# Performance work log

Measured on AMD Instinct MI355X. Metric: run time of the kernel, lower is better.

Reference implementation:

```python
import jax, jax.numpy as jnp
import numpy as np

N_ELEC = 8192   # electrons (nodes)
N_NUC = 512     # nuclei
EMB = 256       # embedding_dim
KER = 256       # kernel_dim
DF = 64         # dist_feat_dim
MID = 128       # round(sqrt(DF*KER)), log-interpolated hidden width of w-MLP
E = 131072      # edges per edge type


def _ssp(x):
    # shifted softplus, deepqmc default activation: log(0.5*exp(x) + 0.5)
    return jax.nn.softplus(x) - jnp.log(2.0)


def setup_inputs() -> dict:
    key = jax.random.key(0)
    ks = jax.random.split(key, 24)
    def nrm(k, shape, scale):
        return jax.random.normal(k, shape, dtype=jnp.float32) * scale
    inp = {}
    inp['electrons'] = nrm(ks[0], (N_ELEC, EMB), 1.0)
    inp['nuclei'] = nrm(ks[1], (N_NUC, KER), 1.0)
    for i, lbl in enumerate(['same', 'anti', 'n']):
        inp[f'dist_{lbl}'] = jax.random.uniform(ks[2 + i], (E, DF), dtype=jnp.float32)
        inp[f'w1_{lbl}'] = nrm(ks[5 + i], (DF, MID), DF ** -0.5)
        inp[f'b1_{lbl}'] = jnp.zeros((MID,), jnp.float32)
        inp[f'w2_{lbl}'] = nrm(ks[8 + i], (MID, KER), MID ** -0.5)
        inp[f'g_{lbl}'] = nrm(ks[11 + i], (KER, EMB), KER ** -0.5)
    inp['h_w'] = nrm(ks[14], (EMB, KER), EMB ** -0.5)
    inp['senders_same'] = jax.random.randint(ks[15], (E,), 0, N_ELEC)
    inp['senders_anti'] = jax.random.randint(ks[16], (E,), 0, N_ELEC)
    inp['senders_n'] = jax.random.randint(ks[17], (E,), 0, N_NUC)
    inp['receivers_same'] = jax.random.randint(ks[18], (E,), 0, N_ELEC)
    inp['receivers_anti'] = jax.random.randint(ks[19], (E,), 0, N_ELEC)
    inp['receivers_n'] = jax.random.randint(ks[20], (E,), 0, N_ELEC)
    return inp


def reference(electrons, nuclei, dist_same, dist_anti, dist_n,
              w1_same, b1_same, w2_same, w1_anti, b1_anti, w2_anti,
              w1_n, b1_n, w2_n, g_same, g_anti, g_n, h_w,
              senders_same, senders_anti, senders_n,
              receivers_same, receivers_anti, receivers_n):
    def w_mlp(d, w1, b1, w2):
        # MLP with ('log', 2) hidden layers: linear+bias -> SSP -> last linear (no bias)
        return _ssp(d @ w1 + b1) @ w2

    # per-edge filters from distance features: [E, KER]
    we_same = w_mlp(dist_same, w1_same, b1_same, w2_same)
    we_anti = w_mlp(dist_anti, w1_anti, b1_anti, w2_anti)
    we_n = w_mlp(dist_n, w1_n, b1_n, w2_n)

    # shared h (single bias-free linear) on gathered sender electrons: [E, KER]
    hx_same = electrons[senders_same] @ h_w
    hx_anti = electrons[senders_anti] @ h_w

    weh_same = we_same * hx_same
    weh_anti = we_anti * hx_anti
    weh_n = we_n * nuclei[senders_n]

    # scatter-sum messages to receiver electrons: [N_ELEC, KER]
    z_same = jax.ops.segment_sum(weh_same, receivers_same, num_segments=N_ELEC)
    z_anti = jax.ops.segment_sum(weh_anti, receivers_anti, num_segments=N_ELEC)
    z_n = jax.ops.segment_sum(weh_n, receivers_n, num_segments=N_ELEC)

    # per-label g (single bias-free linear) + residual update, order matches original
    return electrons + (z_n @ g_n + z_same @ g_same + z_anti @ g_anti)
```

## Files before the change

### kernel.cpp

```cpp
#include <hip/hip_runtime.h>
#include <stdint.h>


#define N_ELEC 8192
#define N_NUC  512
#define EMB    256
#define KER    256
#define DF     64
#define MID    128
#define NEDGE  131072
#define RPS    8256
#define CSTR   272

using u16 = unsigned short;
typedef short short8 __attribute__((ext_vector_type(8)));
typedef float f32x4 __attribute__((ext_vector_type(4)));

__device__ __forceinline__ float bf2f(u16 h) {
  return __uint_as_float(((unsigned)h) << 16);
}
__device__ __forceinline__ u16 f2bf(float f) {
  unsigned u = __float_as_uint(f);
  return (u16)((u + 0x7FFFu + ((u >> 16) & 1u)) >> 16);
}
__device__ __forceinline__ unsigned pkbf(float a, float b) {
  return ((unsigned)f2bf(b) << 16) | (unsigned)f2bf(a);
}
__device__ __forceinline__ float ssp_fast(float x) {
  const float e = __expf(-fabsf(x));
  return fmaxf(x, 0.f) + __logf(fmaf(0.5f, e, 0.5f));
}

__device__ __forceinline__ void stage_tile(const char* g0, long stride,
                                           char* lds, int tid) {
  const int l = tid & 63, w = tid >> 6;
#pragma unroll
  for (int c = 0; c < 2; ++c) {
    const int r = c * 64 + w * 16 + (l >> 2);
    const int cb = (l & 3) * 16;
    const char* g = g0 + (long)r * stride + cb;
    char* dst = lds + c * 4096 + w * 1024;
    __builtin_amdgcn_global_load_lds(
        (const __attribute__((address_space(1))) unsigned*)g,
        (__attribute__((address_space(3))) unsigned*)dst, 16, 0, 0);
  }
}

__device__ __forceinline__ void stage_f32(const float* g0, int stride_e,
                                          int kt, char* lds, int tid) {
#pragma unroll
  for (int k = 0; k < 8; ++k) {
    const int idx2 = k * 256 + tid;
    const int row = idx2 >> 4, cp = idx2 & 15;
    const float2 v = *(const float2*)(g0 + (long)row * stride_e + kt + cp * 2);
    *(unsigned*)(lds + row * 64 + cp * 4) = pkbf(v.x, v.y);
  }
}

template <bool A_F32>
__device__ __forceinline__ void gemm_core(const char* A0, long as_bytes,
                                          const float* Af, int as_elems,
                                          const char* B0, long bs, int K,
                                          char* As, char* Bs, f32x4 acc[4][4],
                                          int tid) {
  const int l = tid & 63, lane15 = l & 15, quad = l >> 4, wv = tid >> 6;
  const int mw = (wv >> 1) * 64, nw = (wv & 1) * 64;
  for (int kt = 0; kt < K; kt += 32) {
    if (A_F32)
      stage_f32(Af, as_elems, kt, As, tid);
    else
      stage_tile(A0 + (long)kt * 2, as_bytes, As, tid);
    stage_tile(B0 + (long)kt * 2, bs, Bs, tid);
    __syncthreads();
    short8 af[4], bf[4];
#pragma unroll
    for (int i = 0; i < 4; ++i) {
      af[i] = *(const short8*)(As + (mw + i * 16 + lane15) * 64 + quad * 16);
      bf[i] = *(const short8*)(Bs + (nw + i * 16 + lane15) * 64 + quad * 16);
    }
#pragma unroll
    for (int mi = 0; mi < 4; ++mi)
#pragma unroll
      for (int ni = 0; ni < 4; ++ni)
        acc[mi][ni] = __builtin_amdgcn_mfma_f32_16x16x32_bf16(
            af[mi], bf[ni], acc[mi][ni], 0, 0, 0);
    __syncthreads();
  }
}

__device__ __forceinline__ void zero_acc(f32x4 acc[4][4]) {
#pragma unroll
  for (int i = 0; i < 4; ++i)
#pragma unroll
    for (int j = 0; j < 4; ++j) acc[i][j] = (f32x4){0.f, 0.f, 0.f, 0.f};
}

__global__ __launch_bounds__(256) void k_zero2(float4* z, int* cnt) {
  const int b = blockIdx.x;
  if (b < 6144)
    z[b * 256 + threadIdx.x] = (float4){0.f, 0.f, 0.f, 0.f};
  else
    cnt[(b - 6144) * 256 + threadIdx.x] = 0;
}

__global__ __launch_bounds__(256) void k_hist(const int* r0, const int* r1,
                                              const int* r2, int* cnt) {
  const int t = blockIdx.z;
  const int* rcv = t == 0 ? r0 : (t == 1 ? r1 : r2);
  const int e = blockIdx.x * 256 + threadIdx.x;
  atomicAdd(&cnt[t * N_ELEC + rcv[e]], 1);
}

__global__ __launch_bounds__(256) void k_scan(const int* cnt, int* rowptr,
                                              int* cursor) {
  const int t = blockIdx.x, tid = threadIdx.x;
  __shared__ int part[256];
  const int* c = cnt + t * N_ELEC;
  int s = 0;
#pragma unroll
  for (int i = 0; i < 32; ++i) s += c[tid * 32 + i];
  part[tid] = s;
  __syncthreads();
  for (int off = 1; off < 256; off <<= 1) {
    int v = (tid >= off) ? part[tid - off] : 0;
    __syncthreads();
    part[tid] += v;
    __syncthreads();
  }
  int run = (tid == 0) ? 0 : part[tid - 1];
  int* rp = rowptr + t * RPS;
  int* cu = cursor + t * N_ELEC;
  for (int i = 0; i < 32; ++i) {
    rp[tid * 32 + i] = run;
    cu[tid * 32 + i] = run;
    run += c[tid * 32 + i];
  }
  if (tid == 255) rp[N_ELEC] = run;
}

__global__ __launch_bounds__(256) void k_place(const int* r0, const int* r1,
                                               const int* r2, const int* s0,
                                               const int* s1, const int* s2,
                                               int* cursor, int* perm,
                                               int* snd_s, int* rcv_s) {
  const int t = blockIdx.z;
  const int* rcv = t == 0 ? r0 : (t == 1 ? r1 : r2);
  const int* snd = t == 0 ? s0 : (t == 1 ? s1 : s2);
  const int e = blockIdx.x * 256 + threadIdx.x;
  const int rr = rcv[e];
  const int pos = atomicAdd(&cursor[t * N_ELEC + rr], 1);
  perm[t * NEDGE + pos] = e;
  snd_s[t * NEDGE + pos] = snd[e];
  rcv_s[t * NEDGE + pos] = rr;
}

__global__ __launch_bounds__(256) void k_prep(
    const float* h_w, const float* w1s, const float* w1a, const float* w1n,
    const float* w2s, const float* w2a, const float* w2n, const float* gs,
    const float* ga, const float* gn, u16* hwT, u16* w1T, u16* w2T, u16* gT) {
  int i = blockIdx.x * 256 + threadIdx.x;
  if (i < 65536) {
    int n = i >> 8, k = i & 255;
    hwT[i] = f2bf(h_w[k * 256 + n]);
    return;
  }
  int j = i - 65536;
  if (j < 24576) {
    int t = j >> 13, jj = j & 8191, n = jj >> 6, k = jj & 63;
    const float* w1 = t == 0 ? w1s : (t == 1 ? w1a : w1n);
    w1T[j] = f2bf(w1[k * 128 + n]);
    return;
  }
  j -= 24576;
  if (j < 98304) {
    int t = j >> 15, jj = j & 32767, n = jj >> 7, k = jj & 127;
    const float* w2 = t == 0 ? w2s : (t == 1 ? w2a : w2n);
    w2T[j] = f2bf(w2[k * 256 + n]);
    return;
  }
  j -= 98304;
  if (j < 196608) {
    int n = j / 768, q = j % 768, t = q >> 8, k = q & 255;
    const float* g = t == 0 ? gs : (t == 1 ? ga : gn);
    gT[j] = f2bf(g[k * 256 + n]);
  }
}

__global__ __launch_bounds__(256) void k_he(const float* elec, const u16* hwT,
                                            u16* he) {
  __shared__ char As[8192], Bs[8192];
  f32x4 acc[4][4];
  zero_acc(acc);
  const int m0 = blockIdx.x * 128, n0 = blockIdx.y * 128;
  gemm_core<true>(nullptr, 0, elec + (long)m0 * 256, 256,
                  (const char*)hwT + (long)n0 * 512, 512, 256, As, Bs, acc,
                  threadIdx.x);
  const int l = threadIdx.x & 63, lane15 = l & 15, quad = l >> 4,
            wv = threadIdx.x >> 6;
  const int mw = (wv >> 1) * 64, nw = (wv & 1) * 64;
#pragma unroll
  for (int mi = 0; mi < 4; ++mi)
#pragma unroll
    for (int r = 0; r < 4; ++r) {
      const int row = m0 + mw + mi * 16 + quad * 4 + r;
#pragma unroll
      for (int ni = 0; ni < 4; ++ni) {
        const int col = n0 + nw + ni * 16 + lane15;
        he[row * 256 + col] = f2bf(acc[mi][ni][r]);
      }
    }
}

__global__ __launch_bounds__(256) void k_edge(
    const float* d0, const float* d1, const float* d2, const float* b0,
    const float* b1p, const float* b2, const u16* w1T, const u16* w2T,
    const u16* he, const float* nucf, const int* perm, const int* snd_s,
    const int* rcv_s, float* z) {
  __shared__ char mid[128 * CSTR];
  __shared__ char buf[128 * CSTR];
  __shared__ int snd_l[128], rcv_l[128];

  const int t = blockIdx.z;
  const int m0 = blockIdx.x * 128;
  const int tid = threadIdx.x;
  const float* dist = t == 0 ? d0 : (t == 1 ? d1 : d2);
  const float* bias = t == 0 ? b0 : (t == 1 ? b1p : b2);
  const u16* w1t = w1T + t * 8192;
  const u16* w2t = w2T + t * 32768;
  const bool is_nuc = (t == 2);

  if (tid < 128)
    snd_l[tid] = snd_s[t * NEDGE + m0 + tid];
  else
    rcv_l[tid - 128] = rcv_s[t * NEDGE + m0 + tid - 128];

  int rows[4];
  const int* pm = perm + t * NEDGE + m0;
#pragma unroll
  for (int s = 0; s < 4; ++s) rows[s] = pm[(s * 256 + tid) >> 3];
#pragma unroll
  for (int j = 0; j < 2; ++j)
#pragma unroll
    for (int s = 0; s < 4; ++s) {
      const int idx = s * 256 + tid, row = idx >> 3, ch = idx & 7;
      const float4 v =
          *(const float4*)(dist + (long)rows[s] * 64 + j * 32 + ch * 4);
      uint2 p;
      p.x = pkbf(v.x, v.y);
      p.y = pkbf(v.z, v.w);
      *(uint2*)(buf + j * 8192 + row * 64 + ch * 8) = p;
    }
  __syncthreads();

  const int l = tid & 63, lane15 = l & 15, quad = l >> 4, wv = tid >> 6;
  const int mw = (wv >> 1) * 64, nw = (wv & 1) * 64;

  f32x4 acc[4][4];
  zero_acc(acc);
#pragma unroll
  for (int j = 0; j < 2; ++j) {
    short8 af[4], bf[4];
#pragma unroll
    for (int i = 0; i < 4; ++i) {
      af[i] = *(const short8*)(buf + j * 8192 + (mw + i * 16 + lane15) * 64 +
                               quad * 16);
      bf[i] = *(const short8*)(w1t + (nw + i * 16 + lane15) * 64 + j * 32 +
                               quad * 8);
    }
#pragma unroll
    for (int mi = 0; mi < 4; ++mi)
#pragma unroll
      for (int ni = 0; ni < 4; ++ni)
        acc[mi][ni] = __builtin_amdgcn_mfma_f32_16x16x32_bf16(
            af[mi], bf[ni], acc[mi][ni], 0, 0, 0);
  }
  __syncthreads();

#pragma unroll
  for (int mi = 0; mi < 4; ++mi)
#pragma unroll
    for (int r = 0; r < 4; ++r) {
      const int row = mw + mi * 16 + quad * 4 + r;
#pragma unroll
      for (int ni = 0; ni < 4; ++ni) {
        const int col = nw + ni * 16 + lane15;
        const float x = acc[mi][ni][r] + bias[col];
        *(u16*)(mid + row * CSTR + col * 2) = f2bf(ssp_fast(x));
      }
    }
  __syncthreads();

  u16* HeC = (u16*)buf;
  for (int n0 = 0; n0 < 256; n0 += 128) {
    zero_acc(acc);
#pragma unroll
    for (int kt = 0; kt < 128; kt += 32) {
      short8 af[4], bf[4];
#pragma unroll
      for (int i = 0; i < 4; ++i) {
        af[i] = *(const short8*)(mid + (mw + i * 16 + lane15) * CSTR + kt * 2 +
                                 quad * 16);
        bf[i] = *(const short8*)(w2t + (n0 + nw + i * 16 + lane15) * 128 + kt +
                                 quad * 8);
      }
#pragma unroll
      for (int mi = 0; mi < 4; ++mi)
#pragma unroll
        for (int ni = 0; ni < 4; ++ni)
          acc[mi][ni] = __builtin_amdgcn_mfma_f32_16x16x32_bf16(
              af[mi], bf[ni], acc[mi][ni], 0, 0, 0);
    }

    if (!is_nuc) {
#pragma unroll
      for (int c = 0; c < 8; ++c) {
        const int chunk = c * 256 + tid;
        const int row = chunk >> 4, off = chunk & 15;
        const uint4 v = *(const uint4*)((const char*)he +
                                        (size_t)snd_l[row] * 512 + n0 * 2 +
                                        off * 16);
        *(uint4*)((char*)HeC + row * CSTR + off * 16) = v;
      }
    } else {
#pragma unroll
      for (int c = 0; c < 8; ++c) {
        const int chunk = c * 256 + tid;
        const int row = chunk >> 4, off = chunk & 15;
        const char* src =
            (const char*)nucf + (size_t)snd_l[row] * 1024 + n0 * 4 + off * 32;
        const float4 a = *(const float4*)src;
        const float4 b = *(const float4*)(src + 16);
        uint4 p;
        p.x = pkbf(a.x, a.y);
        p.y = pkbf(a.z, a.w);
        p.z = pkbf(b.x, b.y);
        p.w = pkbf(b.z, b.w);
        *(uint4*)((char*)HeC + row * CSTR + off * 16) = p;
      }
    }
    __syncthreads();

#pragma unroll
    for (int mi = 0; mi < 4; ++mi)
#pragma unroll
      for (int r = 0; r < 4; ++r) {
        const int row = mw + mi * 16 + quad * 4 + r;
#pragma unroll
        for (int ni = 0; ni < 4; ++ni) {
          const int col = nw + ni * 16 + lane15;
          u16* p = (u16*)((char*)HeC + row * CSTR) + col;
          *p = f2bf(acc[mi][ni][r] * bf2f(*p));
        }
      }
    __syncthreads();

    {
      const int cp = l;
      const int rbeg = wv * 32, rend = rbeg + 32;
      float a0 = 0.f, a1 = 0.f;
      int cur = rcv_l[rbeg];
      for (int row = rbeg; row < rend; ++row) {
        const unsigned p = *(const unsigned*)((char*)HeC + row * CSTR + cp * 4);
        a0 += __uint_as_float(p << 16);
        a1 += __uint_as_float(p & 0xffff0000u);
        const int nxt = (row + 1 < rend) ? rcv_l[row + 1] : -1;
        if (nxt != cur) {
          float* zp = z + (size_t)cur * 768 + t * 256 + n0 + cp * 2;
          unsafeAtomicAdd(zp, a0);
          unsafeAtomicAdd(zp + 1, a1);
          a0 = a1 = 0.f;
          cur = nxt;
        }
      }
    }
    __syncthreads();
  }
}

__global__ __launch_bounds__(256) void k_final(const float* z, const u16* gT,
                                               const float* elec, float* out) {
  __shared__ char As[8192], Bs[8192];
  f32x4 acc[4][4];
  zero_acc(acc);
  const int m0 = blockIdx.x * 128, n0 = blockIdx.y * 128;
  gemm_core<true>(nullptr, 0, z + (long)m0 * 768, 768,
                  (const char*)gT + (long)n0 * 1536, 1536, 768, As, Bs, acc,
                  threadIdx.x);
  const int l = threadIdx.x & 63, lane15 = l & 15, quad = l >> 4,
            wv = threadIdx.x >> 6;
  const int mw = (wv >> 1) * 64, nw = (wv & 1) * 64;
#pragma unroll
  for (int mi = 0; mi < 4; ++mi)
#pragma unroll
    for (int r = 0; r < 4; ++r) {
      const int row = m0 + mw + mi * 16 + quad * 4 + r;
#pragma unroll
      for (int ni = 0; ni < 4; ++ni) {
        const int col = n0 + nw + ni * 16 + lane15;
        out[row * 256 + col] = acc[mi][ni][r] + elec[row * 256 + col];
      }
    }
}

extern "C" void kernel_launch(void* const* d_in, const int* in_sizes, int n_in,
                              void* d_out, int out_size, void* d_ws,
                              size_t ws_size, hipStream_t stream) {
  int I_dist[3], I_w1[3], I_b1[3], I_w2[3], I_g[3], I_hw;
  if (in_sizes[3] == 64 * 128) {
    for (int t = 0; t < 3; ++t) {
      I_dist[t] = 2 + t * 5 + 0;
      I_w1[t] = 2 + t * 5 + 1;
      I_b1[t] = 2 + t * 5 + 2;
      I_w2[t] = 2 + t * 5 + 3;
      I_g[t] = 2 + t * 5 + 4;
    }
    I_hw = 17;
  } else {
    I_dist[0] = 2; I_dist[1] = 3; I_dist[2] = 4;
    I_w1[0] = 5;  I_b1[0] = 6;  I_w2[0] = 7;
    I_w1[1] = 8;  I_b1[1] = 9;  I_w2[1] = 10;
    I_w1[2] = 11; I_b1[2] = 12; I_w2[2] = 13;
    I_g[0] = 14; I_g[1] = 15; I_g[2] = 16;
    I_hw = 17;
  }
  const int I_snd[3] = {18, 19, 20};
  const int I_rcv[3] = {21, 22, 23};

  char* ws = (char*)d_ws;
  u16* he = (u16*)(ws + 0);
  u16* hwT = (u16*)(ws + 4194304);
  u16* w1T = (u16*)(ws + 4325376);
  u16* w2T = (u16*)(ws + 4374528);
  u16* gT = (u16*)(ws + 4571136);
  float* z = (float*)(ws + 4964352);
  int* cnt = (int*)(ws + 30130176);
  int* rowptr = (int*)(ws + 30228480);
  int* cursor = (int*)(ws + 30327552);
  int* perm = (int*)(ws + 30425856);
  int* snd_s = (int*)(ws + 31998720);
  int* rcv_s = (int*)(ws + 33571584);

  const float* elec = (const float*)d_in[0];
  const float* nuc = (const float*)d_in[1];
  const int* s0 = (const int*)d_in[I_snd[0]];
  const int* s1 = (const int*)d_in[I_snd[1]];
  const int* s2 = (const int*)d_in[I_snd[2]];
  const int* r0 = (const int*)d_in[I_rcv[0]];
  const int* r1 = (const int*)d_in[I_rcv[1]];
  const int* r2 = (const int*)d_in[I_rcv[2]];

  k_zero2<<<6240, 256, 0, stream>>>((float4*)z, cnt);

  k_hist<<<dim3(NEDGE / 256, 1, 3), 256, 0, stream>>>(r0, r1, r2, cnt);
  k_scan<<<3, 256, 0, stream>>>(cnt, rowptr, cursor);
  k_place<<<dim3(NEDGE / 256, 1, 3), 256, 0, stream>>>(r0, r1, r2, s0, s1, s2,
                                                       cursor, perm, snd_s,
                                                       rcv_s);

  k_prep<<<1504, 256, 0, stream>>>(
      (const float*)d_in[I_hw], (const float*)d_in[I_w1[0]],
      (const float*)d_in[I_w1[1]], (const float*)d_in[I_w1[2]],
      (const float*)d_in[I_w2[0]], (const float*)d_in[I_w2[1]],
      (const float*)d_in[I_w2[2]], (const float*)d_in[I_g[0]],
      (const float*)d_in[I_g[1]], (const float*)d_in[I_g[2]], hwT, w1T, w2T,
      gT);

  k_he<<<dim3(N_ELEC / 128, 2), 256, 0, stream>>>(elec, hwT, he);

  k_edge<<<dim3(NEDGE / 128, 1, 3), 256, 0, stream>>>(
      (const float*)d_in[I_dist[0]], (const float*)d_in[I_dist[1]],
      (const float*)d_in[I_dist[2]], (const float*)d_in[I_b1[0]],
      (const float*)d_in[I_b1[1]], (const float*)d_in[I_b1[2]], w1T, w2T, he,
      nuc, perm, snd_s, rcv_s, z);

  k_final<<<dim3(N_ELEC / 128, 2), 256, 0, stream>>>(z, gT, elec,
                                                     (float*)d_out);
}
```

Measured before the change: 436.1 us.

## Shrink dense GEMM tiles to 64x64 and cut edge kernel LDS for occupancy

The k_he and k_final GEMMs move from 128x128 to 64x64 tiles, so each launch has four times as many blocks and uses less shared memory per block, which fills more CUs on the 8192-row problems. In k_edge the separate `mid` LDS buffer is removed: the hidden SSP activations are written into `buf`, preloaded into registers (afr) and reused across both n0 halves. A launch bound of 3 blocks per SM is also added. The aim is higher occupancy and less LDS traffic. The cost is more register pressure from holding the A fragments, and less data reuse per block in the smaller GEMM tiles.

```diff
diff --git a/kernel.cpp b/kernel.cpp
--- a/kernel.cpp
+++ b/kernel.cpp
@@ -31,68 +31,56 @@
   return fmaxf(x, 0.f) + __logf(fmaf(0.5f, e, 0.5f));
 }
 
-__device__ __forceinline__ void stage_tile(const char* g0, long stride,
-                                           char* lds, int tid) {
+__device__ __forceinline__ void stage_t64(const char* g0, long stride,
+                                          char* lds, int tid) {
   const int l = tid & 63, w = tid >> 6;
-#pragma unroll
-  for (int c = 0; c < 2; ++c) {
-    const int r = c * 64 + w * 16 + (l >> 2);
-    const int cb = (l & 3) * 16;
-    const char* g = g0 + (long)r * stride + cb;
-    char* dst = lds + c * 4096 + w * 1024;
-    __builtin_amdgcn_global_load_lds(
-        (const __attribute__((address_space(1))) unsigned*)g,
-        (__attribute__((address_space(3))) unsigned*)dst, 16, 0, 0);
-  }
-}
-
-__device__ __forceinline__ void stage_f32(const float* g0, int stride_e,
+  const int r = w * 16 + (l >> 2);
+  const int cb = (l & 3) * 16;
+  __builtin_amdgcn_global_load_lds(
+      (const __attribute__((address_space(1))) unsigned*)(g0 +
+                                                          (long)r * stride +
+                                                          cb),
+      (__attribute__((address_space(3))) unsigned*)(lds + w * 1024), 16, 0, 0);
+}
+__device__ __forceinline__ void stage_f64(const float* g0, int stride_e,
                                           int kt, char* lds, int tid) {
 #pragma unroll
-  for (int k = 0; k < 8; ++k) {
+  for (int k = 0; k < 4; ++k) {
     const int idx2 = k * 256 + tid;
     const int row = idx2 >> 4, cp = idx2 & 15;
     const float2 v = *(const float2*)(g0 + (long)row * stride_e + kt + cp * 2);
     *(unsigned*)(lds + row * 64 + cp * 4) = pkbf(v.x, v.y);
   }
 }
-
 template <bool A_F32>
-__device__ __forceinline__ void gemm_core(const char* A0, long as_bytes,
-                                          const float* Af, int as_elems,
-                                          const char* B0, long bs, int K,
-                                          char* As, char* Bs, f32x4 acc[4][4],
-                                          int tid) {
+__device__ __forceinline__ void gemm64(const char* A0, long as_bytes,
+                                       const float* Af, int as_elems,
+                                       const char* B0, long bs, int K,
+                                       char* As, char* Bs, f32x4 acc[2][2],
+                                       int tid) {
   const int l = tid & 63, lane15 = l & 15, quad = l >> 4, wv = tid >> 6;
-  const int mw = (wv >> 1) * 64, nw = (wv & 1) * 64;
+  const int mw = (wv >> 1) * 32, nw = (wv & 1) * 32;
   for (int kt = 0; kt < K; kt += 32) {
     if (A_F32)
-      stage_f32(Af, as_elems, kt, As, tid);
+      stage_f64(Af, as_elems, kt, As, tid);
     else
-      stage_tile(A0 + (long)kt * 2, as_bytes, As, tid);
-    stage_tile(B0 + (long)kt * 2, bs, Bs, tid);
-    __syncthreads();
-    short8 af[4], bf[4];
-#pragma unroll
-    for (int i = 0; i < 4; ++i) {
+      stage_t64(A0 + (long)kt * 2, as_bytes, As, tid);
+    stage_t64(B0 + (long)kt * 2, bs, Bs, tid);
+    __syncthreads();
+    short8 af[2], bf[2];
+#pragma unroll
+    for (int i = 0; i < 2; ++i) {
       af[i] = *(const short8*)(As + (mw + i * 16 + lane15) * 64 + quad * 16);
       bf[i] = *(const short8*)(Bs + (nw + i * 16 + lane15) * 64 + quad * 16);
     }
 #pragma unroll
-    for (int mi = 0; mi < 4; ++mi)
-#pragma unroll
-      for (int ni = 0; ni < 4; ++ni)
+    for (int mi = 0; mi < 2; ++mi)
+#pragma unroll
+      for (int ni = 0; ni < 2; ++ni)
         acc[mi][ni] = __builtin_amdgcn_mfma_f32_16x16x32_bf16(
             af[mi], bf[ni], acc[mi][ni], 0, 0, 0);
     __syncthreads();
   }
-}
-
-__device__ __forceinline__ void zero_acc(f32x4 acc[4][4]) {
-#pragma unroll
-  for (int i = 0; i < 4; ++i)
-#pragma unroll
-    for (int j = 0; j < 4; ++j) acc[i][j] = (f32x4){0.f, 0.f, 0.f, 0.f};
 }
 
 __global__ __launch_bounds__(256) void k_zero2(float4* z, int* cnt) {
@@ -188,35 +176,37 @@
 
 __global__ __launch_bounds__(256) void k_he(const float* elec, const u16* hwT,
                                             u16* he) {
-  __shared__ char As[8192], Bs[8192];
-  f32x4 acc[4][4];
-  zero_acc(acc);
-  const int m0 = blockIdx.x * 128, n0 = blockIdx.y * 128;
-  gemm_core<true>(nullptr, 0, elec + (long)m0 * 256, 256,
-                  (const char*)hwT + (long)n0 * 512, 512, 256, As, Bs, acc,
-                  threadIdx.x);
+  __shared__ char As[4096], Bs[4096];
+  f32x4 acc[2][2];
+#pragma unroll
+  for (int i = 0; i < 2; ++i)
+#pragma unroll
+    for (int j = 0; j < 2; ++j) acc[i][j] = (f32x4){0.f, 0.f, 0.f, 0.f};
+  const int m0 = blockIdx.x * 64, n0 = blockIdx.y * 64;
+  gemm64<true>(nullptr, 0, elec + (long)m0 * 256, 256,
+               (const char*)hwT + (long)n0 * 512, 512, 256, As, Bs, acc,
+               threadIdx.x);
   const int l = threadIdx.x & 63, lane15 = l & 15, quad = l >> 4,
             wv = threadIdx.x >> 6;
-  const int mw = (wv >> 1) * 64, nw = (wv & 1) * 64;
-#pragma unroll
-  for (int mi = 0; mi < 4; ++mi)
+  const int mw = (wv >> 1) * 32, nw = (wv & 1) * 32;
+#pragma unroll
+  for (int mi = 0; mi < 2; ++mi)
 #pragma unroll
     for (int r = 0; r < 4; ++r) {
       const int row = m0 + mw + mi * 16 + quad * 4 + r;
 #pragma unroll
-      for (int ni = 0; ni < 4; ++ni) {
+      for (int ni = 0; ni < 2; ++ni) {
         const int col = n0 + nw + ni * 16 + lane15;
         he[row * 256 + col] = f2bf(acc[mi][ni][r]);
       }
     }
 }
 
-__global__ __launch_bounds__(256) void k_edge(
+__global__ __launch_bounds__(256, 3) void k_edge(
     const float* d0, const float* d1, const float* d2, const float* b0,
     const float* b1p, const float* b2, const u16* w1T, const u16* w2T,
     const u16* he, const float* nucf, const int* perm, const int* snd_s,
     const int* rcv_s, float* z) {
-  __shared__ char mid[128 * CSTR];
   __shared__ char buf[128 * CSTR];
   __shared__ int snd_l[128], rcv_l[128];
 
@@ -256,7 +246,10 @@
   const int mw = (wv >> 1) * 64, nw = (wv & 1) * 64;
 
   f32x4 acc[4][4];
-  zero_acc(acc);
+#pragma unroll
+  for (int i = 0; i < 4; ++i)
+#pragma unroll
+    for (int j = 0; j < 4; ++j) acc[i][j] = (f32x4){0.f, 0.f, 0.f, 0.f};
 #pragma unroll
   for (int j = 0; j < 2; ++j) {
     short8 af[4], bf[4];
@@ -285,30 +278,39 @@
       for (int ni = 0; ni < 4; ++ni) {
         const int col = nw + ni * 16 + lane15;
         const float x = acc[mi][ni][r] + bias[col];
-        *(u16*)(mid + row * CSTR + col * 2) = f2bf(ssp_fast(x));
-      }
-    }
+        *(u16*)(buf + row * CSTR + col * 2) = f2bf(ssp_fast(x));
+      }
+    }
+  __syncthreads();
+
+  short8 afr[4][4];
+#pragma unroll
+  for (int j = 0; j < 4; ++j)
+#pragma unroll
+    for (int i = 0; i < 4; ++i)
+      afr[j][i] = *(const short8*)(buf + (mw + i * 16 + lane15) * CSTR +
+                                   j * 64 + quad * 16);
   __syncthreads();
 
   u16* HeC = (u16*)buf;
   for (int n0 = 0; n0 < 256; n0 += 128) {
-    zero_acc(acc);
-#pragma unroll
-    for (int kt = 0; kt < 128; kt += 32) {
-      short8 af[4], bf[4];
-#pragma unroll
-      for (int i = 0; i < 4; ++i) {
-        af[i] = *(const short8*)(mid + (mw + i * 16 + lane15) * CSTR + kt * 2 +
-                                 quad * 16);
-        bf[i] = *(const short8*)(w2t + (n0 + nw + i * 16 + lane15) * 128 + kt +
-                                 quad * 8);
-      }
+#pragma unroll
+    for (int i = 0; i < 4; ++i)
+#pragma unroll
+      for (int j = 0; j < 4; ++j) acc[i][j] = (f32x4){0.f, 0.f, 0.f, 0.f};
+#pragma unroll
+    for (int j = 0; j < 4; ++j) {
+      short8 bf[4];
+#pragma unroll
+      for (int i = 0; i < 4; ++i)
+        bf[i] = *(const short8*)(w2t + (n0 + nw + i * 16 + lane15) * 128 +
+                                 j * 32 + quad * 8);
 #pragma unroll
       for (int mi = 0; mi < 4; ++mi)
 #pragma unroll
         for (int ni = 0; ni < 4; ++ni)
           acc[mi][ni] = __builtin_amdgcn_mfma_f32_16x16x32_bf16(
-              af[mi], bf[ni], acc[mi][ni], 0, 0, 0);
+              afr[j][mi], bf[ni], acc[mi][ni], 0, 0, 0);
     }
 
     if (!is_nuc) {
@@ -316,9 +318,9 @@
       for (int c = 0; c < 8; ++c) {
         const int chunk = c * 256 + tid;
         const int row = chunk >> 4, off = chunk & 15;
-        const uint4 v = *(const uint4*)((const char*)he +
-                                        (size_t)snd_l[row] * 512 + n0 * 2 +
-                                        off * 16);
+        const uint4 v =
+            *(const uint4*)((const char*)he + (size_t)snd_l[row] * 512 +
+                            n0 * 2 + off * 16);
         *(uint4*)((char*)HeC + row * CSTR + off * 16) = v;
       }
     } else {
@@ -360,7 +362,8 @@
       float a0 = 0.f, a1 = 0.f;
       int cur = rcv_l[rbeg];
       for (int row = rbeg; row < rend; ++row) {
-        const unsigned p = *(const unsigned*)((char*)HeC + row * CSTR + cp * 4);
+        const unsigned p =
+            *(const unsigned*)((char*)HeC + row * CSTR + cp * 4);
         a0 += __uint_as_float(p << 16);
         a1 += __uint_as_float(p & 0xffff0000u);
         const int nxt = (row + 1 < rend) ? rcv_l[row + 1] : -1;
@@ -379,23 +382,26 @@
 
 __global__ __launch_bounds__(256) void k_final(const float* z, const u16* gT,
                                                const float* elec, float* out) {
-  __shared__ char As[8192], Bs[8192];
-  f32x4 acc[4][4];
-  zero_acc(acc);
-  const int m0 = blockIdx.x * 128, n0 = blockIdx.y * 128;
-  gemm_core<true>(nullptr, 0, z + (long)m0 * 768, 768,
-                  (const char*)gT + (long)n0 * 1536, 1536, 768, As, Bs, acc,
-                  threadIdx.x);
+  __shared__ char As[4096], Bs[4096];
+  f32x4 acc[2][2];
+#pragma unroll
+  for (int i = 0; i < 2; ++i)
+#pragma unroll
+    for (int j = 0; j < 2; ++j) acc[i][j] = (f32x4){0.f, 0.f, 0.f, 0.f};
+  const int m0 = blockIdx.x * 64, n0 = blockIdx.y * 64;
+  gemm64<true>(nullptr, 0, z + (long)m0 * 768, 768,
+               (const char*)gT + (long)n0 * 1536, 1536, 768, As, Bs, acc,
+               threadIdx.x);
   const int l = threadIdx.x & 63, lane15 = l & 15, quad = l >> 4,
             wv = threadIdx.x >> 6;
-  const int mw = (wv >> 1) * 64, nw = (wv & 1) * 64;
-#pragma unroll
-  for (int mi = 0; mi < 4; ++mi)
+  const int mw = (wv >> 1) * 32, nw = (wv & 1) * 32;
+#pragma unroll
+  for (int mi = 0; mi < 2; ++mi)
 #pragma unroll
     for (int r = 0; r < 4; ++r) {
       const int row = m0 + mw + mi * 16 + quad * 4 + r;
 #pragma unroll
-      for (int ni = 0; ni < 4; ++ni) {
+      for (int ni = 0; ni < 2; ++ni) {
         const int col = n0 + nw + ni * 16 + lane15;
         out[row * 256 + col] = acc[mi][ni][r] + elec[row * 256 + col];
       }
@@ -465,7 +471,7 @@
       (const float*)d_in[I_g[1]], (const float*)d_in[I_g[2]], hwT, w1T, w2T,
       gT);
 
-  k_he<<<dim3(N_ELEC / 128, 2), 256, 0, stream>>>(elec, hwT, he);
+  k_he<<<dim3(N_ELEC / 64, 4), 256, 0, stream>>>(elec, hwT, he);
 
   k_edge<<<dim3(NEDGE / 128, 1, 3), 256, 0, stream>>>(
       (const float*)d_in[I_dist[0]], (const float*)d_in[I_dist[1]],
@@ -473,6 +479,6 @@
       (const float*)d_in[I_b1[1]], (const float*)d_in[I_b1[2]], w1T, w2T, he,
       nuc, perm, snd_s, rcv_s, z);
 
-  k_final<<<dim3(N_ELEC / 128, 2), 256, 0, stream>>>(z, gT, elec,
-                                                     (float*)d_out);
-}
+  k_final<<<dim3(N_ELEC / 64, 4), 256, 0, stream>>>(z, gT, elec,
+                                                    (float*)d_out);
+}
```

Measured after the change: 457.0 us. +4.8%, slower.
